# Kernel optimization log

Hardware: AMD Instinct MI355X
Metric: run time of the kernel (lower is better)

Reference implementation:

```python
import jax, jax.numpy as jnp
import numpy as np
import math

D_INPUT = 1024
D_Q = 1024
D_K = 1024
D_V = 1024
D_MODEL = 1024
B, S = 4, 2048


def setup_inputs() -> dict:
    key = jax.random.key(0)
    ks = jax.random.split(key, 9)
    sc = 0.02
    return {
        "x": jax.random.normal(ks[0], (B, S, D_INPUT), dtype=jnp.float32),
        "wq": jax.random.normal(ks[1], (D_INPUT, D_Q), dtype=jnp.float32) * sc,
        "bq": jnp.zeros((D_Q,), dtype=jnp.float32),
        "wk": jax.random.normal(ks[2], (D_INPUT, D_K), dtype=jnp.float32) * sc,
        "bk": jnp.zeros((D_K,), dtype=jnp.float32),
        "wv": jax.random.normal(ks[3], (D_INPUT, D_V), dtype=jnp.float32) * sc,
        "bv": jnp.zeros((D_V,), dtype=jnp.float32),
        "wp": jax.random.normal(ks[4], (D_V, D_MODEL), dtype=jnp.float32) * sc,
        "bp": jnp.zeros((D_MODEL,), dtype=jnp.float32),
    }


def reference(x, wq, bq, wk, bk, wv, bv, wp, bp):
    scale = math.sqrt(D_K)  # NOTE: original MULTIPLIES by sqrt(d_k)
    q = x @ wq + bq  # [B,S,Dq]
    k = x @ wk + bk  # [B,S,Dk]
    v = x @ wv + bv  # [B,S,Dv]
    scores = jnp.einsum('bsd,btd->bst', q, k) * scale
    p_attn = jax.nn.softmax(scores, axis=-1)
    # dropout: inference mode (training=False) -> identity
    context = jnp.einsum('bst,btd->bsd', p_attn, v)
    output = context @ wp + bp
    return (output, p_attn)
```

## Files before the change

### kernel.cpp

```cpp
#include <hip/hip_runtime.h>

typedef unsigned short u16;
typedef short bf16x8 __attribute__((ext_vector_type(8)));
typedef float floatx4 __attribute__((ext_vector_type(4)));

static __device__ __forceinline__ u16 f2bf(float f) {
  unsigned int u = __float_as_uint(f);
  unsigned int lsb = (u >> 16) & 1u;
  u += 0x7FFFu + lsb;
  return (u16)(u >> 16);
}
static __device__ __forceinline__ float bf2f(u16 u) {
  return __uint_as_float(((unsigned int)u) << 16);
}

static __device__ __forceinline__ void gl_lds16(const u16* g, u16* l) {
  __builtin_amdgcn_global_load_lds(
      (const __attribute__((address_space(1))) void*)g,
      (__attribute__((address_space(3))) void*)l, 16, 0, 0);
}

__global__ __launch_bounds__(256)
void prep_all(const float* __restrict__ wq, const float* __restrict__ wk,
              const float* __restrict__ wv, const float* __restrict__ wp,
              const float* __restrict__ bq, const float* __restrict__ bk,
              const float* __restrict__ x,
              u16* __restrict__ qkThi, u16* __restrict__ qkTlo,
              u16* __restrict__ wvThi, u16* __restrict__ wpThi,
              float* __restrict__ bqk,
              u16* __restrict__ xhi, u16* __restrict__ xlo,
              u16* __restrict__ xThi) {
  __shared__ float t[32][33];
  const int z = blockIdx.z;
  const int tid = threadIdx.x;
  const int lr = tid >> 3;
  const int lc = (tid & 7) * 4;

  if (z == 4) {
    if (blockIdx.y == 0 && blockIdx.x < 8) {
      const int i = blockIdx.x * 256 + tid;
      bqk[i] = (i < 1024) ? bq[i] : bk[i - 1024];
    }
    return;
  }

  if (z >= 5) {
    const int r0 = ((z - 5) * 32 + blockIdx.y) * 32;
    const int c0 = blockIdx.x * 32;
    float4 v = *(const float4*)(x + (size_t)(r0 + lr) * 1024 + c0 + lc);
    float f[4] = {v.x, v.y, v.z, v.w};
    t[lr][lc + 0] = v.x; t[lr][lc + 1] = v.y; t[lr][lc + 2] = v.z; t[lr][lc + 3] = v.w;
    u16 ph[4], pl[4];
#pragma unroll
    for (int j = 0; j < 4; j++) {
      ph[j] = f2bf(f[j]);
      pl[j] = f2bf(f[j] - bf2f(ph[j]));
    }
    const size_t o = (size_t)(r0 + lr) * 1024 + c0 + lc;
    *(uint2*)(xhi + o) = *(uint2*)ph;
    *(uint2*)(xlo + o) = *(uint2*)pl;
    __syncthreads();
    u16 pt[4];
#pragma unroll
    for (int j = 0; j < 4; j++) pt[j] = f2bf(t[lc + j][lr]);
    const int b = r0 >> 11, rt = r0 & 2047;
    *(uint2*)(xThi + (size_t)b * (1024 * 2048) + (size_t)(c0 + lr) * 2048 + rt + lc) =
        *(uint2*)pt;
    return;
  }

  const float* in = (z == 0) ? wq : (z == 1) ? wk : (z == 2) ? wv : wp;
  u16* hi = (z == 2) ? wvThi : (z == 3) ? wpThi : (qkThi + (size_t)z * 1024 * 1024);
  u16* lo = (z == 0) ? qkTlo : (z == 1) ? (qkTlo + 1024 * 1024) : (u16*)nullptr;
  const int want_lo = (z < 2);

  const int r0 = blockIdx.y * 32, c0 = blockIdx.x * 32;
  float4 v = *(const float4*)(in + (size_t)(r0 + lr) * 1024 + c0 + lc);
  t[lr][lc + 0] = v.x; t[lr][lc + 1] = v.y; t[lr][lc + 2] = v.z; t[lr][lc + 3] = v.w;
  __syncthreads();
  u16 ph[4], pl[4];
#pragma unroll
  for (int j = 0; j < 4; j++) {
    float f = t[lc + j][lr];
    ph[j] = f2bf(f);
    if (want_lo) pl[j] = f2bf(f - bf2f(ph[j]));
  }
  const size_t o = (size_t)(c0 + lr) * 1024 + r0 + lc;
  *(uint2*)(hi + o) = *(uint2*)ph;
  if (want_lo) *(uint2*)(lo + o) = *(uint2*)pl;
}

template<int BM, int SPLIT, int OM, int HB>
__global__ __launch_bounds__(512, 2)
void gemm8(const u16* __restrict__ Ahi, const u16* __restrict__ Alo,
           const u16* __restrict__ Bhi, const u16* __restrict__ Blo,
           const float* __restrict__ bias,
           void* __restrict__ C0, void* __restrict__ C1,
           void* __restrict__ C2, void* __restrict__ C3,
           int lda, int ldb, int ldc, int NP,
           long long aB, long long bB, long long cB, float scale) {
  constexpr int AF = BM / 32;
  constexpr int ASLOT = BM * 32;
  constexpr int VMS = BM / 128;
  __shared__ __align__(16) u16 As[4 * ASLOT];
  __shared__ __align__(16) u16 Bs[4 * 8192];

  const int gx = gridDim.x, gy = gridDim.y, gz = gridDim.z;
  const int flat = blockIdx.x + gx * (blockIdx.y + gy * blockIdx.z);
  const int nwg = gx * gy * gz;
  const int lg = (flat & 7) * (nwg >> 3) + (flat >> 3);
  const int bx = lg % gx;
  const int by = (lg / gx) % gy;
  const int bz = lg / (gx * gy);

  const int m0 = by * BM, n0 = bx * 256;
  const u16* pAhi = Ahi + (size_t)bz * aB;
  const u16* pAlo = SPLIT ? (Alo + (size_t)bz * aB) : (const u16*)nullptr;
  const u16* pBhi = Bhi + (size_t)bz * bB;
  const u16* pBlo = SPLIT ? (Blo + (size_t)bz * bB) : (const u16*)nullptr;

  const int tid = threadIdx.x;
  const int w = tid >> 6;
  const int L = tid & 63;
  const int rr = L & 15, quad = L >> 4;
  const int wm = (w >> 2) * (BM / 2);
  const int wn = (w & 3) * 64;

  const int rbase = w * 16 + (L >> 2);
  const int coff = (((L & 3) ^ ((L >> 3) & 3)) << 3);
  const size_t arow = (size_t)(m0 + rbase) * lda + coff;
  const size_t brow = (size_t)(n0 + rbase) * ldb + coff;
  u16* const ldA = As + w * 512;
  u16* const ldB = Bs + w * 512;

  const int aoff = ((wm + rr) << 5) + ((quad ^ ((rr >> 1) & 3)) << 3);
  const int boff = ((wn + rr) << 5) + ((quad ^ ((rr >> 1) & 3)) << 3);

  auto stageA = [&](int H) {
    const u16* src;
    int koff;
    if (SPLIT) {
      const int kt = H >> 1;
      src = (kt < 32) ? pAhi : pAlo;
      koff = ((kt & 15) << 6) + ((H & 1) << 5);
    } else {
      src = pAhi;
      koff = H << 5;
    }
    const u16* g = src + arow + koff;
    u16* l = ldA + (H & 3) * ASLOT;
    gl_lds16(g, l);
    if (BM == 256) gl_lds16(g + (size_t)128 * lda, l + 4096);
  };
  auto stageB = [&](int H) {
    const u16* src;
    int koff;
    if (SPLIT) {
      const int kt = H >> 1;
      src = (kt < 16) ? pBhi : (kt < 32) ? pBlo : pBhi;
      koff = ((kt & 15) << 6) + ((H & 1) << 5);
    } else {
      src = pBhi;
      koff = H << 5;
    }
    const u16* g = src + brow + koff;
    u16* l = ldB + (H & 3) * 8192;
    gl_lds16(g, l);
    gl_lds16(g + (size_t)128 * ldb, l + 4096);
  };

  floatx4 acc[AF][4] = {};
  bf16x8 aE[AF], aO[AF], b01E[2], b01O[2], b23[2];

#define RD_SET(slot, A_, B_)                                                   \
  {                                                                            \
    const u16* ab_ = As + ((slot) & 3) * ASLOT + aoff;                         \
    const u16* bb_ = Bs + ((slot) & 3) * 8192 + boff;                          \
    _Pragma("unroll")                                                          \
    for (int i = 0; i < AF; i++) A_[i] = *(const bf16x8*)(ab_ + i * 512);      \
    B_[0] = *(const bf16x8*)(bb_);                                             \
    B_[1] = *(const bf16x8*)(bb_ + 512);                                       \
  }

#define PAIRX(H, AC, B01C, AN, B01N, SB2, SA3, RDN, VM)                        \
  {                                                                            \
    __builtin_amdgcn_sched_barrier(0);                                         \
    {                                                                          \
      const u16* bb_ = Bs + ((H) & 3) * 8192 + boff;                           \
      b23[0] = *(const bf16x8*)(bb_ + 1024);                                   \
      b23[1] = *(const bf16x8*)(bb_ + 1536);                                   \
    }                                                                          \
    if (SB2) stageB((H) + 2);                                                  \
    __builtin_amdgcn_sched_barrier(0);                                         \
    __builtin_amdgcn_s_setprio(1);                                             \
    _Pragma("unroll")                                                          \
    for (int i = 0; i < AF; i++) {                                             \
      acc[i][0] = __builtin_amdgcn_mfma_f32_16x16x32_bf16(AC[i], B01C[0], acc[i][0], 0, 0, 0); \
      acc[i][1] = __builtin_amdgcn_mfma_f32_16x16x32_bf16(AC[i], B01C[1], acc[i][1], 0, 0, 0); \
    }                                                                          \
    __builtin_amdgcn_s_setprio(0);                                             \
    __builtin_amdgcn_sched_barrier(0);                                         \
    if (RDN) RD_SET((H) + 1, AN, B01N);                                        \
    if (SA3) stageA((H) + 3);                                                  \
    __builtin_amdgcn_sched_barrier(0);                                         \
    __builtin_amdgcn_s_setprio(1);                                             \
    _Pragma("unroll")                                                          \
    for (int i = 0; i < AF; i++) {                                             \
      acc[i][2] = __builtin_amdgcn_mfma_f32_16x16x32_bf16(AC[i], b23[0], acc[i][2], 0, 0, 0); \
      acc[i][3] = __builtin_amdgcn_mfma_f32_16x16x32_bf16(AC[i], b23[1], acc[i][3], 0, 0, 0); \
    }                                                                          \
    __builtin_amdgcn_s_setprio(0);                                             \
    if ((VM) == 2) asm volatile("s_waitcnt vmcnt(2)");                         \
    else if ((VM) == 1) asm volatile("s_waitcnt vmcnt(1)");                    \
    else if ((VM) == 0) asm volatile("s_waitcnt vmcnt(0)");                    \
    __builtin_amdgcn_s_barrier();                                              \
  }

  stageA(0); stageB(0); stageA(1); stageB(1); stageA(2);
  if (VMS == 2) asm volatile("s_waitcnt vmcnt(2)");
  else          asm volatile("s_waitcnt vmcnt(1)");
  __builtin_amdgcn_s_barrier();
  RD_SET(0, aE, b01E);

  for (int H = 0; H + 4 < NP; H += 2) {
    PAIRX(H,     aE, b01E, aO, b01O, true, true, true, VMS);
    PAIRX(H + 1, aO, b01O, aE, b01E, true, true, true, VMS);
  }
  {
    const int T = NP - 4;
    PAIRX(T,     aE, b01E, aO, b01O, true,  true,  true,  VMS);
    PAIRX(T + 1, aO, b01O, aE, b01E, true,  false, true,  0);
    PAIRX(T + 2, aE, b01E, aO, b01O, false, false, true,  -1);
    PAIRX(T + 3, aO, b01O, aE, b01E, false, false, false, -1);
  }
#undef PAIRX
#undef RD_SET

#pragma unroll
  for (int i = 0; i < AF; i++) {
    const int mb = m0 + wm + i * 16 + quad * 4;
#pragma unroll
    for (int j = 0; j < 4; j++) {
      const int col = n0 + wn + j * 16 + rr;
      float bvs = 0.f;
      if (HB) bvs = bias[col];
      if (OM == 5) {
        u16* hi; u16* lo;
        if (col < 1024) { hi = (u16*)C0; lo = (u16*)C1; }
        else            { hi = (u16*)C2; lo = (u16*)C3; }
        const int cc = col & 1023;
#pragma unroll
        for (int ii = 0; ii < 4; ii++) {
          const float v = acc[i][j][ii] + bvs;
          const size_t idx = (size_t)(mb + ii) * 1024 + cc;
          const u16 h = f2bf(v);
          hi[idx] = h;
          lo[idx] = f2bf(v - bf2f(h));
        }
      } else if (OM == 0) {
        u16* Cb = (u16*)C0 + (size_t)bz * cB;
#pragma unroll
        for (int ii = 0; ii < 4; ii++) {
          const float v = acc[i][j][ii] * scale + bvs;
          Cb[(size_t)(mb + ii) * ldc + col] = f2bf(v);
        }
      } else {
        float* Cf = (float*)C0 + (size_t)bz * cB;
#pragma unroll
        for (int ii = 0; ii < 4; ii++)
          Cf[(size_t)(mb + ii) * ldc + col] = acc[i][j][ii] * scale + bvs;
      }
    }
  }
}

__global__ __launch_bounds__(256)
void softmax_rows(float* __restrict__ S, u16* __restrict__ Pb) {
  const int row = blockIdx.x;
  float* s = S + (size_t)row * 2048;
  const int tid = threadIdx.x;
  const int w = tid >> 6;
  __shared__ float redm[4];
  __shared__ float reds[4];

  float v[8];
  float mx = -1e30f;
#pragma unroll
  for (int i = 0; i < 8; i++) {
    v[i] = s[tid + 256 * i];
    mx = fmaxf(mx, v[i]);
  }
#pragma unroll
  for (int o = 32; o > 0; o >>= 1) mx = fmaxf(mx, __shfl_xor(mx, o, 64));
  if ((tid & 63) == 0) redm[w] = mx;
  __syncthreads();
  mx = fmaxf(fmaxf(redm[0], redm[1]), fmaxf(redm[2], redm[3]));

  float sum = 0.f;
#pragma unroll
  for (int i = 0; i < 8; i++) {
    v[i] = __expf(v[i] - mx);
    sum += v[i];
  }
#pragma unroll
  for (int o = 32; o > 0; o >>= 1) sum += __shfl_xor(sum, o, 64);
  if ((tid & 63) == 0) reds[w] = sum;
  __syncthreads();
  sum = reds[0] + reds[1] + reds[2] + reds[3];
  const float rs = 1.0f / sum;
#pragma unroll
  for (int i = 0; i < 8; i++) {
    const float p = v[i] * rs;
    s[tid + 256 * i] = p;
    Pb[(size_t)row * 2048 + tid + 256 * i] = f2bf(p);
  }
}

extern "C" void kernel_launch(void* const* d_in, const int* in_sizes, int n_in,
                              void* d_out, int out_size, void* d_ws, size_t ws_size,
                              hipStream_t stream) {
  const float* x  = (const float*)d_in[0];
  const float* wq = (const float*)d_in[1];
  const float* bq = (const float*)d_in[2];
  const float* wk = (const float*)d_in[3];
  const float* bk = (const float*)d_in[4];
  const float* wv = (const float*)d_in[5];
  const float* bv = (const float*)d_in[6];
  const float* wp = (const float*)d_in[7];
  const float* bp = (const float*)d_in[8];

  const size_t MB = 1024 * 1024;
  char* ws = (char*)d_ws;
  u16* qkThi = (u16*)(ws + 0 * MB);
  u16* qkTlo = (u16*)(ws + 4 * MB);
  u16* wvThi = (u16*)(ws + 8 * MB);
  u16* wpThi = (u16*)(ws + 10 * MB);
  float* bqk = (float*)(ws + 12 * MB);
  u16* xhi   = (u16*)(ws + 13 * MB);
  u16* xlo   = (u16*)(ws + 29 * MB);
  u16* qhi   = (u16*)(ws + 45 * MB);
  u16* qlo   = (u16*)(ws + 61 * MB);
  u16* khi   = (u16*)(ws + 77 * MB);
  u16* klo   = (u16*)(ws + 93 * MB);
  u16* xThi  = (u16*)(ws + 109 * MB);
  u16* pbf   = khi;
  u16* px    = qhi;
  u16* ctx   = qlo;

  float* outp = (float*)d_out;
  float* scf  = (float*)d_out + 8388608;

  prep_all<<<dim3(32, 32, 13), dim3(256), 0, stream>>>(
      wq, wk, wv, wp, bq, bk, x, qkThi, qkTlo, wvThi, wpThi, bqk, xhi, xlo, xThi);

  gemm8<256, 1, 5, 1><<<dim3(8, 32, 1), dim3(512), 0, stream>>>(
      xhi, xlo, qkThi, qkTlo, bqk, qhi, qlo, khi, klo,
      1024, 1024, 1024, 96, 0, 0, 0, 1.0f);

  gemm8<256, 1, 2, 0><<<dim3(8, 8, 4), dim3(512), 0, stream>>>(
      qhi, qlo, khi, klo, nullptr, scf, nullptr, nullptr, nullptr,
      1024, 1024, 2048, 96, 2048LL * 1024, 2048LL * 1024, 2048LL * 2048, 32.0f);

  softmax_rows<<<dim3(8192), dim3(256), 0, stream>>>(scf, pbf);

  gemm8<128, 0, 0, 0><<<dim3(4, 16, 4), dim3(512), 0, stream>>>(
      pbf, nullptr, xThi, nullptr, nullptr, px, nullptr, nullptr, nullptr,
      2048, 2048, 1024, 64, 2048LL * 2048, 1024LL * 2048, 2048LL * 1024, 1.0f);

  gemm8<128, 0, 0, 1><<<dim3(4, 64, 1), dim3(512), 0, stream>>>(
      px, nullptr, wvThi, nullptr, bv, ctx, nullptr, nullptr, nullptr,
      1024, 1024, 1024, 32, 0, 0, 0, 1.0f);

  gemm8<128, 0, 2, 1><<<dim3(4, 64, 1), dim3(512), 0, stream>>>(
      ctx, nullptr, wpThi, nullptr, bp, outp, nullptr, nullptr, nullptr,
      1024, 1024, 1024, 32, 0, 0, 0, 1.0f);
}
```

Measured before the change: 439.0 us.

## Restructure GEMM pipeline to single mid-step barrier and joint A/B staging

Reworks the software pipeline in the bf16 MFMA GEMM. The vmcnt wait and workgroup barrier move from the end of each half-step to the middle, between the two MFMA groups. Both A and B tiles are now staged three steps ahead in one place, instead of B two ahead and A three ahead. The aim is to overlap the barrier and global-to-LDS loads with compute better and to simplify the prologue and epilogue. It risks LDS slot reuse hazards with 4-slot buffers and 3-ahead prefetch, and the vmcnt counts must match the number of outstanding loads.

Result: slower. 458.8 us (+4.5%).

```diff
diff --git a/kernel.cpp b/kernel.cpp
--- a/kernel.cpp
+++ b/kernel.cpp
@@ -101,7 +101,7 @@
            long long aB, long long bB, long long cB, float scale) {
   constexpr int AF = BM / 32;
   constexpr int ASLOT = BM * 32;
-  constexpr int VMS = BM / 128;
+  constexpr int L = 2 + BM / 128;
   __shared__ __align__(16) u16 As[4 * ASLOT];
   __shared__ __align__(16) u16 Bs[4 * 8192];
 
@@ -121,13 +121,13 @@
 
   const int tid = threadIdx.x;
   const int w = tid >> 6;
-  const int L = tid & 63;
-  const int rr = L & 15, quad = L >> 4;
+  const int L64 = tid & 63;
+  const int rr = L64 & 15, quad = L64 >> 4;
   const int wm = (w >> 2) * (BM / 2);
   const int wn = (w & 3) * 64;
 
-  const int rbase = w * 16 + (L >> 2);
-  const int coff = (((L & 3) ^ ((L >> 3) & 3)) << 3);
+  const int rbase = w * 16 + (L64 >> 2);
+  const int coff = (((L64 & 3) ^ ((L64 >> 3) & 3)) << 3);
   const size_t arow = (size_t)(m0 + rbase) * lda + coff;
   const size_t brow = (size_t)(n0 + rbase) * ldb + coff;
   u16* const ldA = As + w * 512;
@@ -182,16 +182,17 @@
     B_[1] = *(const bf16x8*)(bb_ + 512);                                       \
   }
 
-#define PAIRX(H, AC, B01C, AN, B01N, SB2, SA3, RDN, VM)                        \
+#define PAIRX(H, AC, B01C, AN, B01N, STG, RDN, VM)                             \
   {                                                                            \
     __builtin_amdgcn_sched_barrier(0);                                         \
+                                                        \
     {                                                                          \
       const u16* bb_ = Bs + ((H) & 3) * 8192 + boff;                           \
       b23[0] = *(const bf16x8*)(bb_ + 1024);                                   \
       b23[1] = *(const bf16x8*)(bb_ + 1536);                                   \
     }                                                                          \
-    if (SB2) stageB((H) + 2);                                                  \
     __builtin_amdgcn_sched_barrier(0);                                         \
+                                                            \
     __builtin_amdgcn_s_setprio(1);                                             \
     _Pragma("unroll")                                                          \
     for (int i = 0; i < AF; i++) {                                             \
@@ -200,9 +201,16 @@
     }                                                                          \
     __builtin_amdgcn_s_setprio(0);                                             \
     __builtin_amdgcn_sched_barrier(0);                                         \
+                               \
+    if ((VM) == 4) asm volatile("s_waitcnt vmcnt(4)");                         \
+    else if ((VM) == 3) asm volatile("s_waitcnt vmcnt(3)");                    \
+    else if ((VM) == 0) asm volatile("s_waitcnt vmcnt(0)");                    \
+    __builtin_amdgcn_s_barrier();                                              \
+                                \
     if (RDN) RD_SET((H) + 1, AN, B01N);                                        \
-    if (SA3) stageA((H) + 3);                                                  \
+    if (STG) { stageA((H) + 3); stageB((H) + 3); }                             \
     __builtin_amdgcn_sched_barrier(0);                                         \
+                                                            \
     __builtin_amdgcn_s_setprio(1);                                             \
     _Pragma("unroll")                                                          \
     for (int i = 0; i < AF; i++) {                                             \
@@ -210,28 +218,24 @@
       acc[i][3] = __builtin_amdgcn_mfma_f32_16x16x32_bf16(AC[i], b23[1], acc[i][3], 0, 0, 0); \
     }                                                                          \
     __builtin_amdgcn_s_setprio(0);                                             \
-    if ((VM) == 2) asm volatile("s_waitcnt vmcnt(2)");                         \
-    else if ((VM) == 1) asm volatile("s_waitcnt vmcnt(1)");                    \
-    else if ((VM) == 0) asm volatile("s_waitcnt vmcnt(0)");                    \
-    __builtin_amdgcn_s_barrier();                                              \
-  }
-
-  stageA(0); stageB(0); stageA(1); stageB(1); stageA(2);
-  if (VMS == 2) asm volatile("s_waitcnt vmcnt(2)");
-  else          asm volatile("s_waitcnt vmcnt(1)");
+  }
+
+  stageA(0); stageB(0); stageA(1); stageB(1); stageA(2); stageB(2);
+  if (L == 4) asm volatile("s_waitcnt vmcnt(8)");
+  else        asm volatile("s_waitcnt vmcnt(6)");
   __builtin_amdgcn_s_barrier();
   RD_SET(0, aE, b01E);
 
   for (int H = 0; H + 4 < NP; H += 2) {
-    PAIRX(H,     aE, b01E, aO, b01O, true, true, true, VMS);
-    PAIRX(H + 1, aO, b01O, aE, b01E, true, true, true, VMS);
+    PAIRX(H,     aE, b01E, aO, b01O, true, true, L);
+    PAIRX(H + 1, aO, b01O, aE, b01E, true, true, L);
   }
   {
     const int T = NP - 4;
-    PAIRX(T,     aE, b01E, aO, b01O, true,  true,  true,  VMS);
-    PAIRX(T + 1, aO, b01O, aE, b01E, true,  false, true,  0);
-    PAIRX(T + 2, aE, b01E, aO, b01O, false, false, true,  -1);
-    PAIRX(T + 3, aO, b01O, aE, b01E, false, false, false, -1);
+    PAIRX(T,     aE, b01E, aO, b01O, true,  true,  L);
+    PAIRX(T + 1, aO, b01O, aE, b01E, false, true,  L);
+    PAIRX(T + 2, aE, b01E, aO, b01O, false, true,  0);
+    PAIRX(T + 3, aO, b01O, aE, b01E, false, false, -1);
   }
 #undef PAIRX
 #undef RD_SET
```
